# Optimization experiments

Hardware: AMD Instinct MI355X
Metric: run time of the kernel (lower is better)

## Reference

```python
import jax, jax.numpy as jnp
import numpy as np

N, E, D = 10000, 640000, 128
H1, H2, OUT = 256, 256, 64
EPS = 1e-5

def _layernorm(h, g, b):
    m = jnp.mean(h, axis=-1, keepdims=True)
    v = jnp.mean((h - m) ** 2, axis=-1, keepdims=True)
    return (h - m) * jax.lax.rsqrt(v + EPS) * g + b

def setup_inputs() -> dict:
    key = jax.random.key(0)
    ks = jax.random.split(key, 20)
    def lin(k, fan_in, fan_out):
        bound = 1.0 / np.sqrt(fan_in)
        kw, kb = jax.random.split(k)
        W = jax.random.uniform(kw, (fan_in, fan_out), jnp.float32, -bound, bound)
        b = jax.random.uniform(kb, (fan_out,), jnp.float32, -bound, bound)
        return W, b
    pool_w, pool_b = lin(ks[0], D, D)
    w1, b1 = lin(ks[1], D, H1)
    w2, b2 = lin(ks[2], H1, H2)
    mu_w, mu_b = lin(ks[3], H2, OUT)
    lv_w, lv_b = lin(ks[4], H2, OUT)
    return {
        "x": jax.random.normal(ks[5], (N, D), jnp.float32),
        "edge_index": jax.random.randint(ks[6], (2, E), 0, N, jnp.int32),
        "edge_strength": jax.random.uniform(ks[7], (E,), jnp.float32),
        "ewmc": jnp.float32(0.5),
        "pool_w": pool_w, "pool_b": pool_b,
        "lnp_g": jnp.ones((D,), jnp.float32), "lnp_b": jnp.zeros((D,), jnp.float32),
        "w1": w1, "b1": b1,
        "ln1_g": jnp.ones((H1,), jnp.float32), "ln1_b": jnp.zeros((H1,), jnp.float32),
        "w2": w2, "b2": b2,
        "ln2_g": jnp.ones((H2,), jnp.float32), "ln2_b": jnp.zeros((H2,), jnp.float32),
        "mu_w": mu_w, "mu_b": mu_b,
        "lv_w": lv_w, "lv_b": lv_b,
    }

def reference(x, edge_index, edge_strength, ewmc, pool_w, pool_b, lnp_g, lnp_b,
              w1, b1, ln1_g, ln1_b, w2, b2, ln2_g, ln2_b, mu_w, mu_b, lv_w, lv_b):
    src, dst = edge_index[0], edge_index[1]
    coef = jax.nn.softplus(ewmc)
    # [E, D] gather + edge scaling
    msgs = x[src] * (1.0 + coef * edge_strength[:, None])
    pooled = jax.nn.relu(_layernorm(msgs @ pool_w + pool_b, lnp_g, lnp_b))
    # segment max by dst; torch_scatter fills empty segments with 0 and pooled >= 0
    agg = jax.ops.segment_max(pooled, dst, num_segments=x.shape[0])
    agg = jnp.maximum(agg, 0.0)
    h = jax.nn.relu(_layernorm(agg @ w1 + b1, ln1_g, ln1_b))
    h = jax.nn.relu(_layernorm(h @ w2 + b2, ln2_g, ln2_b))
    mu = h @ mu_w + mu_b
    logvar = h @ lv_w + lv_b
    std = jnp.exp(0.5 * logvar)
    return (mu, std)
```

## Files before the change

### kernel.cpp

```cpp
#include <hip/hip_runtime.h>
#include <math.h>

#define D_DIM   128
#define H1_DIM  256
#define H2_DIM  256
#define OUT_DIM 64
#define LN_EPS  1e-5f
#define NSHARD  4

typedef __attribute__((ext_vector_type(8))) short bf16x8;
typedef __attribute__((ext_vector_type(4))) float f32x4;

__device__ __forceinline__ unsigned short bf16rne(float v) {
    unsigned int b = __float_as_uint(v);
    return (unsigned short)((b + 0x7FFFu + ((b >> 16) & 1u)) >> 16);
}

union BFPack { unsigned int u[4]; bf16x8 v; };

__global__ __launch_bounds__(512) void k_pool(
        const float* __restrict__ x, const float* __restrict__ pw,
        const float* __restrict__ pb,
        unsigned short* __restrict__ y, float4* __restrict__ stat4,
        const int* __restrict__ ei, int* __restrict__ cnt, int E, int epb,
        const float* __restrict__ w1, const float* __restrict__ w2,
        const float* __restrict__ muw, const float* __restrict__ lvw,
        short* __restrict__ wp1, short* __restrict__ wp2,
        short* __restrict__ wpH) {
    __shared__ __align__(16) short aPack[4 * 64 * 8];
    __shared__ unsigned short yLds[16][128];
    __shared__ float sPart[16][8][3];
    const int tid  = threadIdx.x;
    const int w    = tid >> 6;
    const int lane = tid & 63;
    const int gq   = lane >> 4;
    const int c16  = lane & 15;
    const int row0 = blockIdx.x * 16;

    bf16x8 bfrag[4];
    {
        const int col = w * 16 + c16;
        const int kbase = gq * 8;
#pragma unroll
        for (int kt = 0; kt < 4; ++kt) {
            int k0 = kt * 32 + kbase;
            BFPack t;
#pragma unroll
            for (int jj = 0; jj < 4; ++jj) {
                float a = pw[(k0 + 2 * jj) * D_DIM + col];
                float b = pw[(k0 + 2 * jj + 1) * D_DIM + col];
                t.u[jj] = (unsigned int)bf16rne(a) | ((unsigned int)bf16rne(b) << 16);
            }
            bfrag[kt] = t.v;
        }
    }
    {
        int ebeg = blockIdx.x * epb;
        int eend = ebeg + epb; if (eend > E) eend = E;
        for (int e = ebeg + tid; e < eend; e += 512)
            atomicAdd(&cnt[ei[E + e] * NSHARD + (e & (NSHARD - 1))], 1);
    }
    {
        int r  = tid >> 5;
        int k0 = (tid & 31) * 4;
        float4 v = *(const float4*)&x[(size_t)(row0 + r) * D_DIM + k0];
        int kt = k0 >> 5, sub = (k0 >> 3) & 3, j = k0 & 7;
        int lp = r | (sub << 4);
        unsigned int u0 = (unsigned int)bf16rne(v.x) | ((unsigned int)bf16rne(v.y) << 16);
        unsigned int u1 = (unsigned int)bf16rne(v.z) | ((unsigned int)bf16rne(v.w) << 16);
        *(uint2*)&aPack[kt * 512 + lp * 8 + j] = make_uint2(u0, u1);
    }
    __syncthreads();

    f32x4 A = {0.f, 0.f, 0.f, 0.f};
#pragma unroll
    for (int kt = 0; kt < 4; ++kt) {
        bf16x8 av = *(bf16x8*)&aPack[(kt * 64 + lane) * 8];
        A = __builtin_amdgcn_mfma_f32_16x16x32_bf16(av, bfrag[kt], A, 0, 0, 0);
    }

    {
        float pbf = pb[w * 16 + c16];
#pragma unroll
        for (int r = 0; r < 4; ++r) {
            unsigned short h = bf16rne(A[r]);
            yLds[gq * 4 + r][w * 16 + c16] = h;
            float hf = __uint_as_float((unsigned int)h << 16);
            float s1 = hf, s2 = hf * hf, s3 = hf * pbf;
#pragma unroll
            for (int m = 1; m < 16; m <<= 1) {
                s1 += __shfl_xor(s1, m, 64);
                s2 += __shfl_xor(s2, m, 64);
                s3 += __shfl_xor(s3, m, 64);
            }
            if (c16 == 0) {
                sPart[gq * 4 + r][w][0] = s1;
                sPart[gq * 4 + r][w][1] = s2;
                sPart[gq * 4 + r][w][2] = s3;
            }
        }
    }
    __syncthreads();
    {
        int idx = tid * 4;
        int r = idx >> 7, c = idx & 127;
        *(uint2*)&y[(size_t)(row0 + r) * D_DIM + c] = *(const uint2*)&yLds[r][c];
    }
    if (tid < 16) {
        float t1 = 0.f, t2 = 0.f, t3 = 0.f;
#pragma unroll
        for (int ww = 0; ww < 8; ++ww) {
            t1 += sPart[tid][ww][0]; t2 += sPart[tid][ww][1]; t3 += sPart[tid][ww][2];
        }
        stat4[row0 + tid] = make_float4(t1 * (1.f / 128.f), t2 * (1.f / 128.f),
                                        t3 * (1.f / 128.f), 0.f);
    }
    if (blockIdx.x < 32) {
        int i = blockIdx.x * 512 + tid;
        const float* W; int Ndim, kt, ln, col; short* dst;
        if (i < 4096) {
            int q = i >> 6; ln = i & 63; kt = q & 3; int ct = q >> 2;
            W = w1; Ndim = H1_DIM; col = ct * 16 + (ln & 15); dst = wp1 + i * 8;
        } else if (i < 12288) {
            int i2 = i - 4096; int q = i2 >> 6; ln = i2 & 63; kt = q & 7; int ct = q >> 3;
            W = w2; Ndim = H2_DIM; col = ct * 16 + (ln & 15); dst = wp2 + i2 * 8;
        } else {
            int i3 = i - 12288; int q = i3 >> 6; ln = i3 & 63; kt = q & 7; int ct = q >> 3;
            Ndim = OUT_DIM; dst = wpH + i3 * 8;
            if (ct < 4) { W = muw; col = ct * 16 + (ln & 15); }
            else        { W = lvw; col = (ct - 4) * 16 + (ln & 15); }
        }
        int k0 = kt * 32 + (ln >> 4) * 8;
        unsigned int u[4];
#pragma unroll
        for (int jj = 0; jj < 4; ++jj) {
            float a = W[(k0 + 2 * jj) * Ndim + col];
            float b = W[(k0 + 2 * jj + 1) * Ndim + col];
            u[jj] = (unsigned int)bf16rne(a) | ((unsigned int)bf16rne(b) << 16);
        }
        *(uint4*)dst = make_uint4(u[0], u[1], u[2], u[3]);
    }
}

__global__ __launch_bounds__(1024) void k_scanA(
        const int* __restrict__ cnt, int* __restrict__ offs,
        int* __restrict__ bsum, int N4) {
    __shared__ int part[1024];
    const int t = threadIdx.x;
    const int idx = blockIdx.x * 1024 + t;
    int v = (idx < N4) ? cnt[idx] : 0;
    part[t] = v;
    __syncthreads();
    for (int off = 1; off < 1024; off <<= 1) {
        int n = (t >= off) ? part[t - off] : 0;
        __syncthreads();
        part[t] += n;
        __syncthreads();
    }
    if (idx < N4) offs[idx] = part[t] - v;
    if (t == 1023) bsum[blockIdx.x] = part[t];
}

__global__ __launch_bounds__(64) void k_scanB(
        const int* __restrict__ bsum, int* __restrict__ bbase,
        int* __restrict__ offs, float* __restrict__ consts,
        const float* __restrict__ ewmc, const float* __restrict__ pb,
        int nblk, int N4) {
    const int l = threadIdx.x;
    {
        float v0 = pb[l], v1 = pb[l + 64];
        float s1 = v0 + v1, s2 = v0 * v0 + v1 * v1;
#pragma unroll
        for (int off = 1; off < 64; off <<= 1) {
            s1 += __shfl_xor(s1, off, 64);
            s2 += __shfl_xor(s2, off, 64);
        }
        if (l == 0) {
            float xw = ewmc[0];
            consts[0] = (xw > 30.f) ? xw : log1pf(expf(xw));
            consts[1] = s1 * (1.f / 128.f);
            consts[2] = s2 * (1.f / 128.f);
        }
    }
    int val = (l < nblk) ? bsum[l] : 0;
    int orig = val;
#pragma unroll
    for (int off = 1; off < 64; off <<= 1) {
        int n = __shfl_up(val, off, 64);
        if (l >= off) val += n;
    }
    if (l < nblk) bbase[l] = val - orig;
    if (l == nblk - 1) offs[N4] = val;
}

__global__ __launch_bounds__(1024) void k_scanC(
        int* __restrict__ offs, int* __restrict__ head,
        const int* __restrict__ bbase, int N4) {
    int idx = blockIdx.x * 1024 + threadIdx.x;
    if (idx < N4) {
        int o = offs[idx] + bbase[blockIdx.x];
        offs[idx] = o;
        head[idx] = o;
    }
}

__global__ __launch_bounds__(256) void k_scatter(
        const int* __restrict__ ei, const float* __restrict__ es,
        const float* __restrict__ consts, const float4* __restrict__ stat4,
        int* __restrict__ head, float4* __restrict__ pairs, int E) {
    const float coef = consts[0], mpb = consts[1], mpb2 = consts[2];
    const int tid = threadIdx.x;
    const int e0 = blockIdx.x * 2048 + tid;
    int srcv[8], dstv[8]; float sv[8]; float4 st[8]; int pos[8]; bool ok[8];
#pragma unroll
    for (int u = 0; u < 8; ++u) {
        int e = e0 + u * 256;
        ok[u] = (e < E);
        if (ok[u]) { srcv[u] = ei[e]; dstv[u] = ei[E + e]; sv[u] = es[e]; }
    }
#pragma unroll
    for (int u = 0; u < 8; ++u) if (ok[u]) st[u] = stat4[srcv[u]];
#pragma unroll
    for (int u = 0; u < 8; ++u) if (ok[u]) {
        int e = e0 + u * 256;
        pos[u] = atomicAdd(&head[dstv[u] * NSHARD + (e & (NSHARD - 1))], 1);
    }
#pragma unroll
    for (int u = 0; u < 8; ++u) if (ok[u]) {
        float s = fmaf(coef, sv[u], 1.0f);
        float m   = fmaf(s, st[u].x, mpb);
        float et2 = fmaf(s * s, st[u].y, fmaf(2.f * s, st[u].z, mpb2));
        float inv = rsqrtf(et2 - m * m + LN_EPS);
        pairs[pos[u]] = make_float4(__int_as_float(srcv[u]), s, m, inv);
    }
}

#define GPROC(P, YB)                                                          \
    {                                                                         \
        float s = (P).y, m = (P).z, inv = (P).w;                              \
        float y0 = __uint_as_float((YB).x << 16);                             \
        float y1 = __uint_as_float((YB).x & 0xFFFF0000u);                     \
        float y2 = __uint_as_float((YB).y << 16);                             \
        float y3 = __uint_as_float((YB).y & 0xFFFF0000u);                     \
        float y4 = __uint_as_float((YB).z << 16);                             \
        float y5 = __uint_as_float((YB).z & 0xFFFF0000u);                     \
        float y6 = __uint_as_float((YB).w << 16);                             \
        float y7 = __uint_as_float((YB).w & 0xFFFF0000u);                     \
        mxA.x = fmaxf(mxA.x, fmaf(fmaf(s, y0, pbA.x) - m, inv * gA.x, bA.x)); \
        mxA.y = fmaxf(mxA.y, fmaf(fmaf(s, y1, pbA.y) - m, inv * gA.y, bA.y)); \
        mxA.z = fmaxf(mxA.z, fmaf(fmaf(s, y2, pbA.z) - m, inv * gA.z, bA.z)); \
        mxA.w = fmaxf(mxA.w, fmaf(fmaf(s, y3, pbA.w) - m, inv * gA.w, bA.w)); \
        mxB.x = fmaxf(mxB.x, fmaf(fmaf(s, y4, pbB.x) - m, inv * gB.x, bB.x)); \
        mxB.y = fmaxf(mxB.y, fmaf(fmaf(s, y5, pbB.y) - m, inv * gB.y, bB.y)); \
        mxB.z = fmaxf(mxB.z, fmaf(fmaf(s, y6, pbB.z) - m, inv * gB.z, bB.z)); \
        mxB.w = fmaxf(mxB.w, fmaf(fmaf(s, y7, pbB.w) - m, inv * gB.w, bB.w)); \
    }

__global__ __launch_bounds__(512) void k_gmlp(
        const float4* __restrict__ pairs, const int* __restrict__ offs,
        const unsigned short* __restrict__ y, const float* __restrict__ pb,
        const float* __restrict__ g, const float* __restrict__ b,
        const short* __restrict__ wp1, const short* __restrict__ wp2,
        const short* __restrict__ wpH,
        const float* __restrict__ b1, const float* __restrict__ g1,
        const float* __restrict__ bb1,
        const float* __restrict__ b2, const float* __restrict__ g2,
        const float* __restrict__ bb2,
        const float* __restrict__ mub, const float* __restrict__ lvb,
        float* __restrict__ out, int N) {
    __shared__ __align__(16) short aPack[8 * 64 * 8];
    __shared__ float sPart[16][8][2];
    __shared__ float sM[16], sI[16];
    const int tid  = threadIdx.x;
    const int w    = tid >> 6;
    const int lane = tid & 63;
    const int gq   = lane >> 4;
    const int c16  = lane & 15;
    const int row0 = blockIdx.x * 16;

    {
        const int sub = lane >> 4;
        const int q   = lane & 15;
        const int d0  = q * 8;
        const float4 pbA = *(const float4*)&pb[d0], pbB = *(const float4*)&pb[d0 + 4];
        const float4 gA  = *(const float4*)&g[d0],  gB  = *(const float4*)&g[d0 + 4];
        const float4 bA  = *(const float4*)&b[d0],  bB  = *(const float4*)&b[d0 + 4];
#pragma unroll
        for (int nn = 0; nn < 2; ++nn) {
            const int r = 2 * w + nn;
            const int node = row0 + r;
            float4 mxA = make_float4(-INFINITY, -INFINITY, -INFINITY, -INFINITY);
            float4 mxB = mxA;
            int j = offs[node * NSHARD];
            const int end = offs[node * NSHARD + NSHARD];
            for (; j + 12 <= end; j += 12) {
                float4 p[3]; uint4 yb[3];
#pragma unroll
                for (int u = 0; u < 3; ++u) p[u] = pairs[j + 4 * u + sub];
#pragma unroll
                for (int u = 0; u < 3; ++u)
                    yb[u] = *(const uint4*)&y[(size_t)__float_as_int(p[u].x) * D_DIM + d0];
#pragma unroll
                for (int u = 0; u < 3; ++u) GPROC(p[u], yb[u]);
            }
            for (; j + 4 <= end; j += 4) {
                float4 p = pairs[j + sub];
                uint4 yb = *(const uint4*)&y[(size_t)__float_as_int(p.x) * D_DIM + d0];
                GPROC(p, yb);
            }
            if (j < end) {
                int rem = end - j;
                float4 p = pairs[j + (sub < rem ? sub : 0)];
                uint4 yb = *(const uint4*)&y[(size_t)__float_as_int(p.x) * D_DIM + d0];
                GPROC(p, yb);
            }
            mxA.x = fmaxf(mxA.x, __shfl_xor(mxA.x, 16, 64));
            mxA.y = fmaxf(mxA.y, __shfl_xor(mxA.y, 16, 64));
            mxA.z = fmaxf(mxA.z, __shfl_xor(mxA.z, 16, 64));
            mxA.w = fmaxf(mxA.w, __shfl_xor(mxA.w, 16, 64));
            mxB.x = fmaxf(mxB.x, __shfl_xor(mxB.x, 16, 64));
            mxB.y = fmaxf(mxB.y, __shfl_xor(mxB.y, 16, 64));
            mxB.z = fmaxf(mxB.z, __shfl_xor(mxB.z, 16, 64));
            mxB.w = fmaxf(mxB.w, __shfl_xor(mxB.w, 16, 64));
            mxA.x = fmaxf(mxA.x, __shfl_xor(mxA.x, 32, 64));
            mxA.y = fmaxf(mxA.y, __shfl_xor(mxA.y, 32, 64));
            mxA.z = fmaxf(mxA.z, __shfl_xor(mxA.z, 32, 64));
            mxA.w = fmaxf(mxA.w, __shfl_xor(mxA.w, 32, 64));
            mxB.x = fmaxf(mxB.x, __shfl_xor(mxB.x, 32, 64));
            mxB.y = fmaxf(mxB.y, __shfl_xor(mxB.y, 32, 64));
            mxB.z = fmaxf(mxB.z, __shfl_xor(mxB.z, 32, 64));
            mxB.w = fmaxf(mxB.w, __shfl_xor(mxB.w, 32, 64));
            if (sub == 0) {
                unsigned int u0 = (unsigned int)bf16rne(fmaxf(mxA.x, 0.f))
                                | ((unsigned int)bf16rne(fmaxf(mxA.y, 0.f)) << 16);
                unsigned int u1 = (unsigned int)bf16rne(fmaxf(mxA.z, 0.f))
                                | ((unsigned int)bf16rne(fmaxf(mxA.w, 0.f)) << 16);
                unsigned int u2 = (unsigned int)bf16rne(fmaxf(mxB.x, 0.f))
                                | ((unsigned int)bf16rne(fmaxf(mxB.y, 0.f)) << 16);
                unsigned int u3 = (unsigned int)bf16rne(fmaxf(mxB.z, 0.f))
                                | ((unsigned int)bf16rne(fmaxf(mxB.w, 0.f)) << 16);
                int kt = q >> 2, sfr = q & 3, lp = r | (sfr << 4);
                *(uint4*)&aPack[kt * 512 + lp * 8] = make_uint4(u0, u1, u2, u3);
            }
        }
    }
    __syncthreads();

    const int ct0 = 2 * w, ct1 = 2 * w + 1;
    f32x4 A0 = {0.f, 0.f, 0.f, 0.f}, A1 = {0.f, 0.f, 0.f, 0.f};

#pragma unroll
    for (int kt = 0; kt < 4; ++kt) {
        bf16x8 av = *(bf16x8*)&aPack[(kt * 64 + lane) * 8];
        bf16x8 bv0 = *(const bf16x8*)&wp1[((ct0 * 4 + kt) * 64 + lane) * 8];
        bf16x8 bv1 = *(const bf16x8*)&wp1[((ct1 * 4 + kt) * 64 + lane) * 8];
        A0 = __builtin_amdgcn_mfma_f32_16x16x32_bf16(av, bv0, A0, 0, 0, 0);
        A1 = __builtin_amdgcn_mfma_f32_16x16x32_bf16(av, bv1, A1, 0, 0, 0);
    }
    {
        int col0 = ct0 * 16 + c16, col1 = ct1 * 16 + c16;
        float bias0 = b1[col0], bias1 = b1[col1];
        float v0[4], v1[4];
#pragma unroll
        for (int r = 0; r < 4; ++r) {
            v0[r] = A0[r] + bias0; v1[r] = A1[r] + bias1;
            float s1 = v0[r] + v1[r];
            float s2 = v0[r] * v0[r] + v1[r] * v1[r];
#pragma unroll
            for (int m = 1; m < 16; m <<= 1) {
                s1 += __shfl_xor(s1, m, 64);
                s2 += __shfl_xor(s2, m, 64);
            }
            if (c16 == 0) { sPart[gq * 4 + r][w][0] = s1; sPart[gq * 4 + r][w][1] = s2; }
        }
        __syncthreads();
        if (tid < 16) {
            float t1 = 0.f, t2 = 0.f;
#pragma unroll
            for (int ww = 0; ww < 8; ++ww) { t1 += sPart[tid][ww][0]; t2 += sPart[tid][ww][1]; }
            float m = t1 * (1.f / 256.f);
            sM[tid] = m;
            sI[tid] = rsqrtf(t2 * (1.f / 256.f) - m * m + LN_EPS);
        }
        __syncthreads();
        float gc0 = g1[col0], bc0 = bb1[col0];
        float gc1 = g1[col1], bc1 = bb1[col1];
#pragma unroll
        for (int r = 0; r < 4; ++r) {
            int row = gq * 4 + r;
            float m = sM[row], inv = sI[row];
            float h0 = fmaxf(fmaf((v0[r] - m) * inv, gc0, bc0), 0.f);
            float h1 = fmaxf(fmaf((v1[r] - m) * inv, gc1, bc1), 0.f);
            aPack[(col0 >> 5) * 512 + (row | (((col0 >> 3) & 3) << 4)) * 8 + (col0 & 7)] = (short)bf16rne(h0);
            aPack[(col1 >> 5) * 512 + (row | (((col1 >> 3) & 3) << 4)) * 8 + (col1 & 7)] = (short)bf16rne(h1);
        }
    }
    __syncthreads();

    A0 = (f32x4){0.f, 0.f, 0.f, 0.f}; A1 = (f32x4){0.f, 0.f, 0.f, 0.f};
#pragma unroll
    for (int kt = 0; kt < 8; ++kt) {
        bf16x8 av = *(bf16x8*)&aPack[(kt * 64 + lane) * 8];
        bf16x8 bv0 = *(const bf16x8*)&wp2[((ct0 * 8 + kt) * 64 + lane) * 8];
        bf16x8 bv1 = *(const bf16x8*)&wp2[((ct1 * 8 + kt) * 64 + lane) * 8];
        A0 = __builtin_amdgcn_mfma_f32_16x16x32_bf16(av, bv0, A0, 0, 0, 0);
        A1 = __builtin_amdgcn_mfma_f32_16x16x32_bf16(av, bv1, A1, 0, 0, 0);
    }
    {
        int col0 = ct0 * 16 + c16, col1 = ct1 * 16 + c16;
        float bias0 = b2[col0], bias1 = b2[col1];
        float v0[4], v1[4];
#pragma unroll
        for (int r = 0; r < 4; ++r) {
            v0[r] = A0[r] + bias0; v1[r] = A1[r] + bias1;
            float s1 = v0[r] + v1[r];
            float s2 = v0[r] * v0[r] + v1[r] * v1[r];
#pragma unroll
            for (int m = 1; m < 16; m <<= 1) {
                s1 += __shfl_xor(s1, m, 64);
                s2 += __shfl_xor(s2, m, 64);
            }
            if (c16 == 0) { sPart[gq * 4 + r][w][0] = s1; sPart[gq * 4 + r][w][1] = s2; }
        }
        __syncthreads();
        if (tid < 16) {
            float t1 = 0.f, t2 = 0.f;
#pragma unroll
            for (int ww = 0; ww < 8; ++ww) { t1 += sPart[tid][ww][0]; t2 += sPart[tid][ww][1]; }
            float m = t1 * (1.f / 256.f);
            sM[tid] = m;
            sI[tid] = rsqrtf(t2 * (1.f / 256.f) - m * m + LN_EPS);
        }
        __syncthreads();
        float gc0 = g2[col0], bc0 = bb2[col0];
        float gc1 = g2[col1], bc1 = bb2[col1];
#pragma unroll
        for (int r = 0; r < 4; ++r) {
            int row = gq * 4 + r;
            float m = sM[row], inv = sI[row];
            float h0 = fmaxf(fmaf((v0[r] - m) * inv, gc0, bc0), 0.f);
            float h1 = fmaxf(fmaf((v1[r] - m) * inv, gc1, bc1), 0.f);
            aPack[(col0 >> 5) * 512 + (row | (((col0 >> 3) & 3) << 4)) * 8 + (col0 & 7)] = (short)bf16rne(h0);
            aPack[(col1 >> 5) * 512 + (row | (((col1 >> 3) & 3) << 4)) * 8 + (col1 & 7)] = (short)bf16rne(h1);
        }
    }
    __syncthreads();

    {
        f32x4 H = {0.f, 0.f, 0.f, 0.f};
#pragma unroll
        for (int kt = 0; kt < 8; ++kt) {
            bf16x8 av = *(bf16x8*)&aPack[(kt * 64 + lane) * 8];
            bf16x8 bv = *(const bf16x8*)&wpH[((w * 8 + kt) * 64 + lane) * 8];
            H = __builtin_amdgcn_mfma_f32_16x16x32_bf16(av, bv, H, 0, 0, 0);
        }
        int colh = (w & 3) * 16 + c16;
        if (w < 4) {
            float bias = mub[colh];
#pragma unroll
            for (int r = 0; r < 4; ++r)
                out[(size_t)(row0 + gq * 4 + r) * OUT_DIM + colh] = H[r] + bias;
        } else {
            float bias = lvb[colh];
#pragma unroll
            for (int r = 0; r < 4; ++r)
                out[(size_t)N * OUT_DIM + (size_t)(row0 + gq * 4 + r) * OUT_DIM + colh] =
                    expf(0.5f * (H[r] + bias));
        }
    }
}

extern "C" void kernel_launch(void* const* d_in, const int* in_sizes, int n_in,
                              void* d_out, int out_size, void* d_ws, size_t ws_size,
                              hipStream_t stream) {
    const float* x      = (const float*)d_in[0];
    const int*   ei     = (const int*)  d_in[1];
    const float* es     = (const float*)d_in[2];
    const float* ewmc   = (const float*)d_in[3];
    const float* pool_w = (const float*)d_in[4];
    const float* pool_b = (const float*)d_in[5];
    const float* lnp_g  = (const float*)d_in[6];
    const float* lnp_b  = (const float*)d_in[7];
    const float* w1     = (const float*)d_in[8];
    const float* b1     = (const float*)d_in[9];
    const float* ln1_g  = (const float*)d_in[10];
    const float* ln1_b  = (const float*)d_in[11];
    const float* w2     = (const float*)d_in[12];
    const float* b2     = (const float*)d_in[13];
    const float* ln2_g  = (const float*)d_in[14];
    const float* ln2_b  = (const float*)d_in[15];
    const float* mu_w   = (const float*)d_in[16];
    const float* mu_b   = (const float*)d_in[17];
    const float* lv_w   = (const float*)d_in[18];
    const float* lv_b   = (const float*)d_in[19];

    const int N  = in_sizes[0] / D_DIM;
    const int E  = in_sizes[2];
    const int N4 = N * NSHARD;
    const int nblkScan = (N4 + 1023) / 1024;

    float*  ws     = (float*)d_ws;
    float*  consts = ws;
    float4* stat4  = (float4*)(ws + 16);
    unsigned short* y = (unsigned short*)(ws + 16 + 4 * (size_t)N);
    size_t  w      = 16 + 4 * (size_t)N + (size_t)N * D_DIM / 2;
    int*    cnt    = (int*)(ws + w); w += N4;
    int*    offs   = (int*)(ws + w); w += N4 + 1;
    int*    head   = (int*)(ws + w); w += N4;
    int*    bsum   = (int*)(ws + w); w += 64;
    int*    bbase  = (int*)(ws + w); w += 64;
    w = (w + 3) & ~(size_t)3;
    short*  wp1    = (short*)(ws + w); w += 16384;
    short*  wp2    = (short*)(ws + w); w += 32768;
    short*  wpH    = (short*)(ws + w); w += 16384;
    float4* pairs  = (float4*)(ws + w);

    const int nbPool = N / 16;
    const int epb    = (E + nbPool - 1) / nbPool;

    hipMemsetAsync(cnt, 0, (size_t)N4 * sizeof(int), stream);
    k_pool<<<nbPool, 512, 0, stream>>>(x, pool_w, pool_b, y, stat4, ei, cnt, E,
                                       epb, w1, w2, mu_w, lv_w, wp1, wp2, wpH);
    k_scanA<<<nblkScan, 1024, 0, stream>>>(cnt, offs, bsum, N4);
    k_scanB<<<1, 64, 0, stream>>>(bsum, bbase, offs, consts, ewmc, pool_b,
                                  nblkScan, N4);
    k_scanC<<<nblkScan, 1024, 0, stream>>>(offs, head, bbase, N4);
    k_scatter<<<(E + 2047) / 2048, 256, 0, stream>>>(ei, es, consts, stat4,
                                                     head, pairs, E);
    k_gmlp<<<N / 16, 512, 0, stream>>>(pairs, offs, y, pool_b, lnp_g, lnp_b,
                                       wp1, wp2, wpH,
                                       b1, ln1_g, ln1_b,
                                       b2, ln2_g, ln2_b,
                                       mu_b, lv_b, (float*)d_out, N);
}
```

Measured before the change: 128.6 us.

## Split fused gather+MLP kernel into separate gather and MLP kernels

The fused gather/MLP kernel is split in two. A new gather kernel uses one wavefront per node (4 nodes per 256-thread block) and writes the aggregated bf16 rows to a global buffer in the MFMA-packed layout. A separate MLP kernel then reads that buffer directly instead of using LDS. The aim is finer-grained parallelism and better load balance for the irregular segment-max gather, and keeping MLP register pressure away from the gather. The cost is an extra launch and a global round-trip of the aggregated activations.

```diff
diff --git a/kernel.cpp b/kernel.cpp
--- a/kernel.cpp
+++ b/kernel.cpp
@@ -7,6 +7,7 @@
 #define OUT_DIM 64
 #define LN_EPS  1e-5f
 #define NSHARD  4
+#define AGGP_STRIDE 2048
 
 typedef __attribute__((ext_vector_type(8))) short bf16x8;
 typedef __attribute__((ext_vector_type(4))) float f32x4;
@@ -256,10 +257,78 @@
         mxB.w = fmaxf(mxB.w, fmaf(fmaf(s, y7, pbB.w) - m, inv * gB.w, bB.w)); \
     }
 
-__global__ __launch_bounds__(512) void k_gmlp(
+__global__ __launch_bounds__(256) void k_gather(
         const float4* __restrict__ pairs, const int* __restrict__ offs,
         const unsigned short* __restrict__ y, const float* __restrict__ pb,
         const float* __restrict__ g, const float* __restrict__ b,
+        unsigned short* __restrict__ aggP, int N) {
+    const int node = blockIdx.x * 4 + (threadIdx.x >> 6);
+    if (node >= N) return;
+    const int lane = threadIdx.x & 63;
+    const int sub  = lane >> 4;
+    const int q    = lane & 15;
+    const int d0   = q * 8;
+    const float4 pbA = *(const float4*)&pb[d0], pbB = *(const float4*)&pb[d0 + 4];
+    const float4 gA  = *(const float4*)&g[d0],  gB  = *(const float4*)&g[d0 + 4];
+    const float4 bA  = *(const float4*)&b[d0],  bB  = *(const float4*)&b[d0 + 4];
+    float4 mxA = make_float4(-INFINITY, -INFINITY, -INFINITY, -INFINITY);
+    float4 mxB = mxA;
+    int j = offs[node * NSHARD];
+    const int end = offs[node * NSHARD + NSHARD];
+    for (; j + 12 <= end; j += 12) {
+        float4 p[3]; uint4 yb[3];
+#pragma unroll
+        for (int u = 0; u < 3; ++u) p[u] = pairs[j + 4 * u + sub];
+#pragma unroll
+        for (int u = 0; u < 3; ++u)
+            yb[u] = *(const uint4*)&y[(size_t)__float_as_int(p[u].x) * D_DIM + d0];
+#pragma unroll
+        for (int u = 0; u < 3; ++u) GPROC(p[u], yb[u]);
+    }
+    for (; j + 4 <= end; j += 4) {
+        float4 p = pairs[j + sub];
+        uint4 yb = *(const uint4*)&y[(size_t)__float_as_int(p.x) * D_DIM + d0];
+        GPROC(p, yb);
+    }
+    if (j < end) {
+        int rem = end - j;
+        float4 p = pairs[j + (sub < rem ? sub : 0)];
+        uint4 yb = *(const uint4*)&y[(size_t)__float_as_int(p.x) * D_DIM + d0];
+        GPROC(p, yb);
+    }
+    mxA.x = fmaxf(mxA.x, __shfl_xor(mxA.x, 16, 64));
+    mxA.y = fmaxf(mxA.y, __shfl_xor(mxA.y, 16, 64));
+    mxA.z = fmaxf(mxA.z, __shfl_xor(mxA.z, 16, 64));
+    mxA.w = fmaxf(mxA.w, __shfl_xor(mxA.w, 16, 64));
+    mxB.x = fmaxf(mxB.x, __shfl_xor(mxB.x, 16, 64));
+    mxB.y = fmaxf(mxB.y, __shfl_xor(mxB.y, 16, 64));
+    mxB.z = fmaxf(mxB.z, __shfl_xor(mxB.z, 16, 64));
+    mxB.w = fmaxf(mxB.w, __shfl_xor(mxB.w, 16, 64));
+    mxA.x = fmaxf(mxA.x, __shfl_xor(mxA.x, 32, 64));
+    mxA.y = fmaxf(mxA.y, __shfl_xor(mxA.y, 32, 64));
+    mxA.z = fmaxf(mxA.z, __shfl_xor(mxA.z, 32, 64));
+    mxA.w = fmaxf(mxA.w, __shfl_xor(mxA.w, 32, 64));
+    mxB.x = fmaxf(mxB.x, __shfl_xor(mxB.x, 32, 64));
+    mxB.y = fmaxf(mxB.y, __shfl_xor(mxB.y, 32, 64));
+    mxB.z = fmaxf(mxB.z, __shfl_xor(mxB.z, 32, 64));
+    mxB.w = fmaxf(mxB.w, __shfl_xor(mxB.w, 32, 64));
+    if (sub == 0) {
+        unsigned int u0 = (unsigned int)bf16rne(fmaxf(mxA.x, 0.f))
+                        | ((unsigned int)bf16rne(fmaxf(mxA.y, 0.f)) << 16);
+        unsigned int u1 = (unsigned int)bf16rne(fmaxf(mxA.z, 0.f))
+                        | ((unsigned int)bf16rne(fmaxf(mxA.w, 0.f)) << 16);
+        unsigned int u2 = (unsigned int)bf16rne(fmaxf(mxB.x, 0.f))
+                        | ((unsigned int)bf16rne(fmaxf(mxB.y, 0.f)) << 16);
+        unsigned int u3 = (unsigned int)bf16rne(fmaxf(mxB.z, 0.f))
+                        | ((unsigned int)bf16rne(fmaxf(mxB.w, 0.f)) << 16);
+        int kt = q >> 2, sfr = q & 3, lp = (node & 15) | (sfr << 4);
+        *(uint4*)&aggP[(size_t)(node >> 4) * AGGP_STRIDE + kt * 512 + lp * 8] =
+            make_uint4(u0, u1, u2, u3);
+    }
+}
+
+__global__ __launch_bounds__(512) void k_mlp(
+        const unsigned short* __restrict__ aggP,
         const short* __restrict__ wp1, const short* __restrict__ wp2,
         const short* __restrict__ wpH,
         const float* __restrict__ b1, const float* __restrict__ g1,
@@ -277,81 +346,14 @@
     const int gq   = lane >> 4;
     const int c16  = lane & 15;
     const int row0 = blockIdx.x * 16;
-
-    {
-        const int sub = lane >> 4;
-        const int q   = lane & 15;
-        const int d0  = q * 8;
-        const float4 pbA = *(const float4*)&pb[d0], pbB = *(const float4*)&pb[d0 + 4];
-        const float4 gA  = *(const float4*)&g[d0],  gB  = *(const float4*)&g[d0 + 4];
-        const float4 bA  = *(const float4*)&b[d0],  bB  = *(const float4*)&b[d0 + 4];
-#pragma unroll
-        for (int nn = 0; nn < 2; ++nn) {
-            const int r = 2 * w + nn;
-            const int node = row0 + r;
-            float4 mxA = make_float4(-INFINITY, -INFINITY, -INFINITY, -INFINITY);
-            float4 mxB = mxA;
-            int j = offs[node * NSHARD];
-            const int end = offs[node * NSHARD + NSHARD];
-            for (; j + 12 <= end; j += 12) {
-                float4 p[3]; uint4 yb[3];
-#pragma unroll
-                for (int u = 0; u < 3; ++u) p[u] = pairs[j + 4 * u + sub];
-#pragma unroll
-                for (int u = 0; u < 3; ++u)
-                    yb[u] = *(const uint4*)&y[(size_t)__float_as_int(p[u].x) * D_DIM + d0];
-#pragma unroll
-                for (int u = 0; u < 3; ++u) GPROC(p[u], yb[u]);
-            }
-            for (; j + 4 <= end; j += 4) {
-                float4 p = pairs[j + sub];
-                uint4 yb = *(const uint4*)&y[(size_t)__float_as_int(p.x) * D_DIM + d0];
-                GPROC(p, yb);
-            }
-            if (j < end) {
-                int rem = end - j;
-                float4 p = pairs[j + (sub < rem ? sub : 0)];
-                uint4 yb = *(const uint4*)&y[(size_t)__float_as_int(p.x) * D_DIM + d0];
-                GPROC(p, yb);
-            }
-            mxA.x = fmaxf(mxA.x, __shfl_xor(mxA.x, 16, 64));
-            mxA.y = fmaxf(mxA.y, __shfl_xor(mxA.y, 16, 64));
-            mxA.z = fmaxf(mxA.z, __shfl_xor(mxA.z, 16, 64));
-            mxA.w = fmaxf(mxA.w, __shfl_xor(mxA.w, 16, 64));
-            mxB.x = fmaxf(mxB.x, __shfl_xor(mxB.x, 16, 64));
-            mxB.y = fmaxf(mxB.y, __shfl_xor(mxB.y, 16, 64));
-            mxB.z = fmaxf(mxB.z, __shfl_xor(mxB.z, 16, 64));
-            mxB.w = fmaxf(mxB.w, __shfl_xor(mxB.w, 16, 64));
-            mxA.x = fmaxf(mxA.x, __shfl_xor(mxA.x, 32, 64));
-            mxA.y = fmaxf(mxA.y, __shfl_xor(mxA.y, 32, 64));
-            mxA.z = fmaxf(mxA.z, __shfl_xor(mxA.z, 32, 64));
-            mxA.w = fmaxf(mxA.w, __shfl_xor(mxA.w, 32, 64));
-            mxB.x = fmaxf(mxB.x, __shfl_xor(mxB.x, 32, 64));
-            mxB.y = fmaxf(mxB.y, __shfl_xor(mxB.y, 32, 64));
-            mxB.z = fmaxf(mxB.z, __shfl_xor(mxB.z, 32, 64));
-            mxB.w = fmaxf(mxB.w, __shfl_xor(mxB.w, 32, 64));
-            if (sub == 0) {
-                unsigned int u0 = (unsigned int)bf16rne(fmaxf(mxA.x, 0.f))
-                                | ((unsigned int)bf16rne(fmaxf(mxA.y, 0.f)) << 16);
-                unsigned int u1 = (unsigned int)bf16rne(fmaxf(mxA.z, 0.f))
-                                | ((unsigned int)bf16rne(fmaxf(mxA.w, 0.f)) << 16);
-                unsigned int u2 = (unsigned int)bf16rne(fmaxf(mxB.x, 0.f))
-                                | ((unsigned int)bf16rne(fmaxf(mxB.y, 0.f)) << 16);
-                unsigned int u3 = (unsigned int)bf16rne(fmaxf(mxB.z, 0.f))
-                                | ((unsigned int)bf16rne(fmaxf(mxB.w, 0.f)) << 16);
-                int kt = q >> 2, sfr = q & 3, lp = r | (sfr << 4);
-                *(uint4*)&aPack[kt * 512 + lp * 8] = make_uint4(u0, u1, u2, u3);
-            }
-        }
-    }
-    __syncthreads();
+    const unsigned short* aG = aggP + (size_t)blockIdx.x * AGGP_STRIDE;
 
     const int ct0 = 2 * w, ct1 = 2 * w + 1;
     f32x4 A0 = {0.f, 0.f, 0.f, 0.f}, A1 = {0.f, 0.f, 0.f, 0.f};
 
 #pragma unroll
     for (int kt = 0; kt < 4; ++kt) {
-        bf16x8 av = *(bf16x8*)&aPack[(kt * 64 + lane) * 8];
+        bf16x8 av = *(const bf16x8*)&aG[(kt * 64 + lane) * 8];
         bf16x8 bv0 = *(const bf16x8*)&wp1[((ct0 * 4 + kt) * 64 + lane) * 8];
         bf16x8 bv1 = *(const bf16x8*)&wp1[((ct1 * 4 + kt) * 64 + lane) * 8];
         A0 = __builtin_amdgcn_mfma_f32_16x16x32_bf16(av, bv0, A0, 0, 0, 0);
@@ -502,8 +504,9 @@
     float*  ws     = (float*)d_ws;
     float*  consts = ws;
     float4* stat4  = (float4*)(ws + 16);
-    unsigned short* y = (unsigned short*)(ws + 16 + 4 * (size_t)N);
-    size_t  w      = 16 + 4 * (size_t)N + (size_t)N * D_DIM / 2;
+    unsigned short* y    = (unsigned short*)(ws + 16 + 4 * (size_t)N);
+    unsigned short* aggP = y + (size_t)N * D_DIM;
+    size_t  w      = 16 + 4 * (size_t)N + (size_t)N * D_DIM;
     int*    cnt    = (int*)(ws + w); w += N4;
     int*    offs   = (int*)(ws + w); w += N4 + 1;
     int*    head   = (int*)(ws + w); w += N4;
@@ -527,9 +530,10 @@
     k_scanC<<<nblkScan, 1024, 0, stream>>>(offs, head, bbase, N4);
     k_scatter<<<(E + 2047) / 2048, 256, 0, stream>>>(ei, es, consts, stat4,
                                                      head, pairs, E);
-    k_gmlp<<<N / 16, 512, 0, stream>>>(pairs, offs, y, pool_b, lnp_g, lnp_b,
-                                       wp1, wp2, wpH,
-                                       b1, ln1_g, ln1_b,
-                                       b2, ln2_g, ln2_b,
-                                       mu_b, lv_b, (float*)d_out, N);
-}
+    k_gather<<<(N + 3) / 4, 256, 0, stream>>>(pairs, offs, y,
+                                              pool_b, lnp_g, lnp_b, aggP, N);
+    k_mlp<<<N / 16, 512, 0, stream>>>(aggP, wp1, wp2, wpH,
+                                      b1, ln1_g, ln1_b,
+                                      b2, ln2_g, ln2_b,
+                                      mu_b, lv_b, (float*)d_out, N);
+}
```

Measured after the change: 116.5 us, median of 2. -9.4%, faster.
